# Optimization experiments

Hardware: AMD Instinct MI355X
Metric: run time of the kernel (lower is better)

Reference implementation:

```python
import jax, jax.numpy as jnp
import numpy as np

N_MEL = 80; ARNN = 1024; ADIM = 128; EMB = 512; PRE = 256; DRNN = 1024; NF = 32; KS = 31
B = 32; NCTX = 512; T = 500
PAD = (KS - 1) // 2


def setup_inputs() -> dict:
    key = jax.random.key(0)
    ks = jax.random.split(key, 20)
    g = lambda k, shape: jax.random.normal(k, shape, dtype=jnp.float32) * 0.02
    return {
        "memory": jax.random.normal(ks[0], (B, NCTX, EMB), dtype=jnp.float32),
        "decoder_inputs": jax.random.normal(ks[1], (B, N_MEL, T), dtype=jnp.float32),
        "mask": jnp.zeros((B, NCTX), dtype=bool),
        "prenet_w1": g(ks[2], (PRE, N_MEL)),
        "prenet_w2": g(ks[3], (PRE, PRE)),
        "arnn_wih": g(ks[4], (4 * ARNN, PRE + EMB)),
        "arnn_whh": g(ks[5], (4 * ARNN, ARNN)),
        "arnn_bih": jnp.zeros((4 * ARNN,), jnp.float32),
        "arnn_bhh": jnp.zeros((4 * ARNN,), jnp.float32),
        "q_w": g(ks[6], (ADIM, ARNN)),
        "m_w": g(ks[7], (ADIM, EMB)),
        "loc_conv_w": g(ks[8], (NF, 2, KS)),
        "loc_w": g(ks[9], (ADIM, NF)),
        "v_w": g(ks[10], (ADIM,)),
        "drnn_wih": g(ks[11], (4 * DRNN, ARNN + EMB)),
        "drnn_whh": g(ks[12], (4 * DRNN, DRNN)),
        "drnn_bih": jnp.zeros((4 * DRNN,), jnp.float32),
        "drnn_bhh": jnp.zeros((4 * DRNN,), jnp.float32),
        "proj_w": g(ks[13], (N_MEL, DRNN + EMB)),
        "proj_b": jnp.zeros((N_MEL,), jnp.float32),
        "gate_w": g(ks[14], (1, DRNN + EMB)),
        "gate_b": jnp.zeros((1,), jnp.float32),
    }


def _lstm_cell(x, h, c, wih, whh, bih, bhh):
    # PyTorch LSTMCell gate order: i, f, g, o
    z = x @ wih.T + h @ whh.T + bih + bhh
    i, f, g, o = jnp.split(z, 4, axis=-1)
    c2 = jax.nn.sigmoid(f) * c + jax.nn.sigmoid(i) * jnp.tanh(g)
    h2 = jax.nn.sigmoid(o) * jnp.tanh(c2)
    return h2, c2


def reference(memory, decoder_inputs, mask,
              prenet_w1, prenet_w2,
              arnn_wih, arnn_whh, arnn_bih, arnn_bhh,
              q_w, m_w, loc_conv_w, loc_w, v_w,
              drnn_wih, drnn_whh, drnn_bih, drnn_bhh,
              proj_w, proj_b, gate_w, gate_b):
    b, n_ctx, emb = memory.shape
    n_mel, t_out = decoder_inputs.shape[1], decoder_inputs.shape[2]

    # (time, batch, n_mel) with a leading zero go-frame; PreNet (eval: no dropout)
    x = jnp.transpose(decoder_inputs, (2, 0, 1))
    x = jnp.concatenate([jnp.zeros((1, b, n_mel), x.dtype), x], axis=0)
    h = jax.nn.relu(x @ prenet_w1.T)
    h = jax.nn.relu(h @ prenet_w2.T)  # (T+1, B, PRE)
    inputs = h[:-1]  # T decoder steps

    proc_mem = memory @ m_w.T  # (B, n_ctx, ADIM)

    def step(carry, xin):
        ah, ac, dh, dc, aw, awc, actx = carry
        cell_in = jnp.concatenate([xin, actx], axis=-1)
        ah, ac = _lstm_cell(cell_in, ah, ac, arnn_wih, arnn_whh, arnn_bih, arnn_bhh)
        # location-sensitive attention
        aw_cat = jnp.stack([aw, awc], axis=1)  # (B, 2, n_ctx)
        loc = jax.lax.conv_general_dilated(
            aw_cat, loc_conv_w, window_strides=(1,), padding=[(PAD, PAD)],
            dimension_numbers=("NCH", "OIH", "NCH"))  # (B, NF, n_ctx)
        loc = jnp.transpose(loc, (0, 2, 1)) @ loc_w.T  # (B, n_ctx, ADIM)
        q = (ah @ q_w.T)[:, None, :]  # (B, 1, ADIM)
        e = jnp.tanh(q + proc_mem + loc) @ v_w  # (B, n_ctx)
        e = jnp.where(mask, -1e9, e)
        aw = jax.nn.softmax(e, axis=-1)
        actx = jnp.einsum("bn,bne->be", aw, memory)
        awc = awc + aw
        din = jnp.concatenate([ah, actx], axis=-1)
        dh, dc = _lstm_cell(din, dh, dc, drnn_wih, drnn_whh, drnn_bih, drnn_bhh)
        dhc = jnp.concatenate([dh, actx], axis=-1)
        mel = dhc @ proj_w.T + proj_b  # (B, n_mel)
        gate = dhc @ gate_w.T + gate_b  # (B, 1)
        return (ah, ac, dh, dc, aw, awc, actx), (mel, gate[:, 0])

    z32 = lambda *s: jnp.zeros(s, memory.dtype)
    carry0 = (z32(b, ARNN), z32(b, ARNN), z32(b, DRNN), z32(b, DRNN),
              z32(b, n_ctx), z32(b, n_ctx), z32(b, emb))
    _, (mels, gates) = jax.lax.scan(step, carry0, inputs)
    mel_out = jnp.transpose(mels, (1, 2, 0))   # (B, n_mel, T)
    gate_out = jnp.transpose(gates, (1, 0))    # (B, T)
    return mel_out, gate_out
```

## Files before the change

kernel.cpp:

```cpp
#include <hip/hip_runtime.h>

#define NBLK 256
#define NTHR 512

constexpr int kNMel = 80, kArnn = 1024, kAdim = 128, kEmb = 512, kPre = 256;
constexpr int kNF = 32, kKS = 31, kB = 32, kNctx = 512, kT = 500, kPad = 15;

constexpr int KT_A = 56;
constexpr int KT_D = 80;
constexpr int KT_ALL = KT_A + KT_D;

constexpr int OFF_PREB   = 0;
constexpr int OFF_PROCMB = OFF_PREB + kT * kB * kPre / 2;
constexpr int OFF_QWTB   = OFF_PROCMB + kB * kNctx * kAdim / 2;
constexpr int OFF_LWT    = OFF_QWTB + kAdim * kArnn / 2;
constexpr int OFF_STATE  = OFF_LWT + kAdim * 33;
constexpr int OFF_AHB    = OFF_STATE;
constexpr int OFF_DHB    = OFF_AHB + 2 * kB * kArnn / 2;
constexpr int OFF_DH     = OFF_DHB + 2 * kB * kArnn / 2;
constexpr int OFF_AC     = OFF_DH + 2 * kB * kArnn;
constexpr int OFF_DC     = OFF_AC + kB * kArnn;
constexpr int OFF_ACTX   = OFF_DC + kB * kArnn;
constexpr int OFF_AW     = OFF_ACTX + kB * kEmb;
constexpr int OFF_AWC    = OFF_AW + kB * kNctx;
constexpr int OFF_PAW    = OFF_AWC + kB * kNctx;
constexpr int OFF_NUM    = OFF_PAW + kB * kNctx;
constexpr int OFF_DEN    = OFF_NUM + 2 * kB * kEmb;
constexpr int OFF_END    = OFF_DEN + 2 * kB;
constexpr int STATE_SZ   = OFF_END - OFF_STATE;
constexpr int OFF_BAR    = OFF_END;
constexpr int BAR_LINES  = 266;
constexpr int OFF_PAN    = OFF_BAR + BAR_LINES * 32;
constexpr int PAN_SZ     = NBLK * KT_ALL * 256;
constexpr int OFF_GMB    = OFF_PAN + PAN_SZ;
constexpr int GMB_SZ     = kB * kNctx * kEmb / 2;

typedef __attribute__((ext_vector_type(4))) float fvec4;
typedef __attribute__((ext_vector_type(8))) short bh8_t;
typedef unsigned long long u64;
typedef unsigned short ushortt;

union U64u { u64 u; float2 f2; ushortt s[4]; };

union SMem {
  struct { ushortt xs[8][2][2048]; } x1;
  struct { float zra[4][2][64][4]; float zrd[4][2][64][4];
           float hb[2][32][4]; } x2;
  struct { float ahb_s[kArnn]; float vw_s[kAdim]; float psum[512]; float q_s[kAdim];
           float aw_s[96]; float awc_s[96]; float cw[kNF * 2 * kKS];
           float loc_s[64 * 33]; float p_s[64]; float lwt[kAdim * 33];
           float dhc[kArnn + kEmb]; float pprj[126];
           ushortt pm[64 * kAdim]; } b;
  struct { float x8[8][80]; float h1[8][256]; } p;
  struct { float mem_s[4][512]; } m;
};

__device__ __forceinline__ float sigf(float x) { return 1.0f / (1.0f + __expf(-x)); }
__device__ __forceinline__ float tanhfast(float x) { return 1.0f - 2.0f / (__expf(2.0f * x) + 1.0f); }

__device__ __forceinline__ ushortt bf16rn(float f) {
  unsigned u = __float_as_uint(f);
  unsigned r = (u + 0x7FFFu + ((u >> 16) & 1u)) >> 16;
  return (ushortt)r;
}
__device__ __forceinline__ float bf2f(ushortt v) {
  return __uint_as_float((unsigned)v << 16);
}

__device__ __forceinline__ u64 ald64(const void* p) {
  return __hip_atomic_load((const u64*)p, __ATOMIC_RELAXED, __HIP_MEMORY_SCOPE_AGENT);
}
__device__ __forceinline__ float alf(const float* p) {
  return __hip_atomic_load(p, __ATOMIC_RELAXED, __HIP_MEMORY_SCOPE_AGENT);
}
__device__ __forceinline__ void asf(float* p, float v) {
  __hip_atomic_store(p, v, __ATOMIC_RELAXED, __HIP_MEMORY_SCOPE_AGENT);
}
__device__ __forceinline__ void as64(void* p, u64 v) {
  __hip_atomic_store((u64*)p, v, __ATOMIC_RELAXED, __HIP_MEMORY_SCOPE_AGENT);
}
__device__ __forceinline__ unsigned alu(const unsigned* p) {
  return __hip_atomic_load(p, __ATOMIC_RELAXED, __HIP_MEMORY_SCOPE_AGENT);
}
__device__ __forceinline__ void asu(unsigned* p, unsigned v) {
  __hip_atomic_store(p, v, __ATOMIC_RELAXED, __HIP_MEMORY_SCOPE_AGENT);
}

__device__ __forceinline__ void gbar_full(unsigned* cnt, unsigned* gen, unsigned& genv) {
  __syncthreads();
  if (threadIdx.x == 0) {
    __threadfence();
    unsigned arrived = __hip_atomic_fetch_add(cnt, 1u, __ATOMIC_ACQ_REL, __HIP_MEMORY_SCOPE_AGENT) + 1u;
    if (arrived == (unsigned)NBLK) {
      __hip_atomic_store(cnt, 0u, __ATOMIC_RELAXED, __HIP_MEMORY_SCOPE_AGENT);
      __hip_atomic_fetch_add(gen, 1u, __ATOMIC_ACQ_REL, __HIP_MEMORY_SCOPE_AGENT);
    } else {
      while (__hip_atomic_load(gen, __ATOMIC_ACQUIRE, __HIP_MEMORY_SCOPE_AGENT) == genv) {
        __builtin_amdgcn_s_sleep(2);
      }
    }
    ++genv;
  }
  __syncthreads();
}

__device__ __forceinline__ void gbar_light(unsigned* bar, unsigned target, int bk, int tid) {
  asm volatile("s_waitcnt vmcnt(0) lgkmcnt(0)" ::: "memory");
  __syncthreads();
  if (bk == 0) {
    if (tid < 64) {
      if (tid == 0) {
        asm volatile("s_waitcnt vmcnt(0)" ::: "memory");
      }
      unsigned i1 = (unsigned)tid * 4 + 1, i2 = i1 + 1, i3 = i1 + 2;
      unsigned i0 = (unsigned)tid * 4;
      for (;;) {
        bool ok = true;
        if (i0 != 0) ok = ok && (alu(&bar[i0 * 32]) >= target);
        ok = ok && (alu(&bar[i1 * 32]) >= target);
        ok = ok && (alu(&bar[i2 * 32]) >= target);
        ok = ok && (alu(&bar[i3 * 32]) >= target);
        if (__all(ok)) break;
        __builtin_amdgcn_s_sleep(1);
      }
      if (tid < 8) asu(&bar[(256 + tid) * 32], target);
    }
  } else {
    if (tid == 0) {
      asm volatile("s_waitcnt vmcnt(0)" ::: "memory");
      asu(&bar[bk * 32], target);
      unsigned* wk = &bar[(256 + (bk & 7)) * 32];
      while (alu(wk) < target) __builtin_amdgcn_s_sleep(1);
    }
  }
  __syncthreads();
}

template<int LS, int W>
__device__ __forceinline__ void lstm_wave(
    const ushortt* __restrict__ s0, const ushortt* __restrict__ s2,
    const float* __restrict__ numq, const float* __restrict__ invden,
    const short* __restrict__ pan,
    int l, ushortt* xstg, fvec4& z0, fvec4& z1)
{
  constexpr int NC  = LS ? 10 : 7;
  constexpr int CB  = LS ? W * 640 : W * 448;
  constexpr int KT0 = LS ? W * 20 : W * 14;
  constexpr int BD0 = LS ? 1024 : 256;
  constexpr int BD1 = LS ? 1536 : 768;
  const int u8 = l & 15, rj = l >> 4;
  const int m = l & 15, kg = l >> 4;

  u64 L0[8], L1[8];
  bh8_t f00, f01, f10, f11;

  auto load = [&](int c, u64* L, bh8_t& f0, bh8_t& f1) {
    const int c0 = CB + c * 64;
    if (c0 >= BD0 && c0 < BD1) {
      const float* base = numq + (c0 - BD0) + u8 * 4;
      #pragma unroll
      for (int j = 0; j < 8; ++j) {
        int row = 4 * j + rj;
        const float* fp = base + (size_t)row * kEmb;
        U64u a, b2; a.u = ald64(fp); b2.u = ald64(fp + 2);
        float s = invden[row];
        U64u pk;
        pk.s[0] = bf16rn(a.f2.x * s);  pk.s[1] = bf16rn(a.f2.y * s);
        pk.s[2] = bf16rn(b2.f2.x * s); pk.s[3] = bf16rn(b2.f2.y * s);
        L[j] = pk.u;
      }
    } else {
      const ushortt* bsrc; int stride; bool coh;
      if (c0 < BD0) { bsrc = s0 + c0;       stride = (LS ? 1024 : 256); coh = (LS == 1); }
      else          { bsrc = s2 + c0 - BD1; stride = 1024;              coh = true; }
      #pragma unroll
      for (int j = 0; j < 8; ++j) {
        const ushortt* ap = bsrc + (size_t)(4 * j + rj) * stride + u8 * 4;
        L[j] = coh ? ald64(ap) : *reinterpret_cast<const u64*>(ap);
      }
    }
    f0 = *reinterpret_cast<const bh8_t*>(pan + (size_t)(KT0 + c * 2) * 512 + l * 8);
    f1 = *reinterpret_cast<const bh8_t*>(pan + (size_t)(KT0 + c * 2 + 1) * 512 + l * 8);
  };
  auto stash = [&](int buf, u64* L) {
    #pragma unroll
    for (int j = 0; j < 8; ++j) {
      int row = 4 * j + rj;
      int sw = u8 ^ ((row & 7) << 1);
      *reinterpret_cast<u64*>(xstg + buf * 2048 + row * 64 + sw * 4) = L[j];
    }
  };
  auto consume = [&](int buf, bh8_t f0, bh8_t f1) {
    #pragma unroll
    for (int kt = 0; kt < 2; ++kt) {
      int sw = (2 * (kt * 4 + kg)) ^ ((m & 7) << 1);
      bh8_t a0 = *reinterpret_cast<const bh8_t*>(xstg + buf * 2048 + m * 64 + sw * 4);
      bh8_t a1 = *reinterpret_cast<const bh8_t*>(xstg + buf * 2048 + (16 + m) * 64 + sw * 4);
      bh8_t f = kt ? f1 : f0;
      z0 = __builtin_amdgcn_mfma_f32_16x16x32_bf16(a0, f, z0, 0, 0, 0);
      z1 = __builtin_amdgcn_mfma_f32_16x16x32_bf16(a1, f, z1, 0, 0, 0);
    }
  };

  load(0, L0, f00, f01);
  #pragma unroll
  for (int c = 0; c < NC; c += 2) {
    stash(0, L0);
    if (c + 1 < NC) load(c + 1, L1, f10, f11);
    consume(0, f00, f01);
    if (c + 1 < NC) {
      stash(1, L1);
      if (c + 2 < NC) load(c + 2, L0, f00, f01);
      consume(1, f10, f11);
    }
  }
}

extern "C" __global__ void __launch_bounds__(NTHR, 1)
decoder_kernel(const float* __restrict__ gmem, const float* __restrict__ dec,
               const unsigned char* __restrict__ mask,
               const float* __restrict__ pw1, const float* __restrict__ pw2,
               const float* __restrict__ awih, const float* __restrict__ awhh,
               const float* __restrict__ abih, const float* __restrict__ abhh,
               const float* __restrict__ qw, const float* __restrict__ mw,
               const float* __restrict__ cvw, const float* __restrict__ locw,
               const float* __restrict__ vw,
               const float* __restrict__ dwih, const float* __restrict__ dwhh,
               const float* __restrict__ dbih, const float* __restrict__ dbhh,
               const float* __restrict__ pjw, const float* __restrict__ pjb,
               const float* __restrict__ gw, const float* __restrict__ gb,
               float* __restrict__ out, float* __restrict__ ws, int useg)
{
  __shared__ SMem sm;
  __shared__ float s_invden[32];
  const int bk = blockIdx.x, tid = threadIdx.x;
  unsigned genv_f = 0, bcnt = 0;
  unsigned* bar = reinterpret_cast<unsigned*>(ws + OFF_BAR);
  unsigned* cntF = &bar[264 * 32];
  unsigned* genF = &bar[265 * 32];

  ushortt* PREBu = reinterpret_cast<ushortt*>(ws + OFF_PREB);
  ushortt* PROCMBu = reinterpret_cast<ushortt*>(ws + OFF_PROCMB);
  ushortt* QWTBu = reinterpret_cast<ushortt*>(ws + OFF_QWTB);
  float* LWT = ws + OFF_LWT;
  ushortt* AHBu = reinterpret_cast<ushortt*>(ws + OFF_AHB);
  ushortt* DHBu = reinterpret_cast<ushortt*>(ws + OFF_DHB);
  float* DH = ws + OFF_DH;
  float* AC = ws + OFF_AC;
  float* DC = ws + OFF_DC;
  float* ACTX = ws + OFF_ACTX;
  float* AWp = ws + OFF_AW;
  float* AWC = ws + OFF_AWC;
  float* PAW = ws + OFF_PAW;
  float* NUM = ws + OFF_NUM;
  float* DEN = ws + OFF_DEN;
  short* PANS = reinterpret_cast<short*>(ws + OFF_PAN);
  ushortt* GMB = reinterpret_cast<ushortt*>(ws + OFF_GMB);

  for (int i = bk * NTHR + tid; i < STATE_SZ; i += NBLK * NTHR) (ws + OFF_STATE)[i] = 0.f;
  for (int i = bk * NTHR + tid; i < kAdim * kArnn; i += NBLK * NTHR)
    QWTBu[i] = bf16rn(qw[i]);
  for (int i = bk * NTHR + tid; i < kAdim * kNF; i += NBLK * NTHR) {
    int d = i >> 5, f = i & 31;
    LWT[d * 33 + f] = locw[i];
  }
  gbar_full(cntF, genF, genv_f);

  if (bk == 0 && tid < 2 * kB) asf(&DEN[tid], 1.0f);
  for (int it = 0; it < 16; ++it) {
    int task0 = bk * 64 + it * 4;
    for (int i = tid; i < 2048; i += NTHR) {
      int pr = i >> 9, h = i & 511;
      sm.m.mem_s[pr][h] = gmem[(size_t)(task0 + pr) * kEmb + h];
    }
    __syncthreads();
    {
      int pr = tid >> 7, d = tid & 127;
      const float* mwr = mw + d * kEmb;
      float acc = 0.f;
      for (int h = 0; h < kEmb; ++h) acc = fmaf(sm.m.mem_s[pr][h], mwr[h], acc);
      PROCMBu[(size_t)(task0 + pr) * kAdim + d] = bf16rn(acc);
    }
    if (useg) {
      for (int i = tid; i < 2048; i += NTHR) {
        int pr = i >> 9, h = i & 511;
        GMB[(size_t)(task0 + pr) * kEmb + h] = bf16rn(sm.m.mem_s[pr][h]);
      }
    }
    __syncthreads();
  }
  for (int g = bk; g < 2000; g += NBLK) {
    int t_idx = g >> 2;
    int b0 = (g & 3) * 8;
    if (t_idx == 0) {
      for (int i = tid; i < 8 * kPre; i += NTHR)
        PREBu[(size_t)(b0 + (i >> 8)) * kPre + (i & 255)] = 0;
      continue;
    }
    for (int i = tid; i < 640; i += NTHR) {
      int bb = i / 80, m2 = i % 80;
      sm.p.x8[bb][m2] = dec[((size_t)(b0 + bb) * kNMel + m2) * kT + (t_idx - 1)];
    }
    __syncthreads();
    {
      int u = tid & 255, rep = tid >> 8;
      float acc[4] = {0.f, 0.f, 0.f, 0.f};
      for (int m2 = 0; m2 < 80; ++m2) {
        float w = pw1[u * kNMel + m2];
        #pragma unroll
        for (int r = 0; r < 4; ++r) acc[r] = fmaf(w, sm.p.x8[rep * 4 + r][m2], acc[r]);
      }
      #pragma unroll
      for (int r = 0; r < 4; ++r) sm.p.h1[rep * 4 + r][u] = fmaxf(acc[r], 0.f);
    }
    __syncthreads();
    {
      int u = tid & 255, rep = tid >> 8;
      float acc[4] = {0.f, 0.f, 0.f, 0.f};
      for (int k = 0; k < kPre; ++k) {
        float w = pw2[u * kPre + k];
        #pragma unroll
        for (int r = 0; r < 4; ++r) acc[r] = fmaf(w, sm.p.h1[rep * 4 + r][k], acc[r]);
      }
      #pragma unroll
      for (int r = 0; r < 4; ++r)
        PREBu[((size_t)t_idx * kB + b0 + rep * 4 + r) * kPre + u] = bf16rn(fmaxf(acc[r], 0.f));
    }
    __syncthreads();
  }
  {
    const int UNITS = NBLK * KT_ALL * 64;
    for (int u = bk * NTHR + tid; u < UNITS; u += NBLK * NTHR) {
      int bkk = u / (KT_ALL * 64);
      int rem = u - bkk * (KT_ALL * 64);
      int kta = rem >> 6, l = rem & 63;
      int lstm = (kta >= KT_A);
      int kt = lstm ? kta - KT_A : kta;
      int n = l & 15, kg = l >> 4;
      int r = (n >> 2) * 1024 + bkk * 4 + (n & 3);
      bh8_t v;
      #pragma unroll
      for (int j = 0; j < 8; ++j) {
        int k = kt * 32 + kg * 8 + j;
        float wv;
        if (!lstm) wv = (k < 768) ? awih[(size_t)r * 768 + k] : awhh[(size_t)r * 1024 + (k - 768)];
        else       wv = (k < 1536) ? dwih[(size_t)r * 1536 + k] : dwhh[(size_t)r * 1024 + (k - 1536)];
        v[j] = (short)bf16rn(wv);
      }
      *reinterpret_cast<bh8_t*>(PANS + (size_t)u * 8) = v;
    }
  }
  gbar_full(cntF, genF, genv_f);

  for (int t = 0; t <= kT; ++t) {
    const int p = t & 1, q = p ^ 1;
    float* nump = NUM + p * kB * kEmb;
    const float* numq = NUM + q * kB * kEmb;

    if (tid < kB) s_invden[tid] = 1.0f / alf(DEN + q * kB + tid);
    __syncthreads();
    if (t > 0 && tid < 64) {
      int idx = bk * 64 + tid;
      int b2 = idx >> 9;
      float invd = s_invden[b2];
      float av = PAW[idx] * invd;
      asf(&AWp[idx], av);
      asf(&AWC[idx], alf(&AWC[idx]) + av);
      asf(&ACTX[idx], alf(&numq[idx]) * invd);
    }
    if (t < kT) {
      if (tid < 64) asf(&nump[bk * 64 + tid], 0.f);
      if (bk == 0 && tid < kB) asf(DEN + p * kB + tid, 0.f);
    }
    {
      const int w8 = tid >> 6, l = tid & 63;
      fvec4 z0 = {0.f, 0.f, 0.f, 0.f}, z1 = z0;
      const ushortt* AHBq_ = AHBu + q * kB * kArnn;
      const ushortt* DHBp_ = DHBu + p * kB * kArnn;
      const ushortt* preb_t = PREBu + (size_t)t * kB * kPre;
      ushortt* xst = &sm.x1.xs[w8][0][0];
      const short* panb = PANS + (size_t)bk * (KT_ALL * 512);
      const short* pand = panb + KT_A * 512;
      if (w8 < 4) {
        if (t < kT) {
          switch (w8) {
            case 0: lstm_wave<0,0>(preb_t, AHBq_, numq, s_invden, panb, l, xst, z0, z1); break;
            case 1: lstm_wave<0,1>(preb_t, AHBq_, numq, s_invden, panb, l, xst, z0, z1); break;
            case 2: lstm_wave<0,2>(preb_t, AHBq_, numq, s_invden, panb, l, xst, z0, z1); break;
            default: lstm_wave<0,3>(preb_t, AHBq_, numq, s_invden, panb, l, xst, z0, z1); break;
          }
        }
      } else {
        if (t > 0) {
          switch (w8) {
            case 4: lstm_wave<1,0>(AHBq_, DHBp_, numq, s_invden, pand, l, xst, z0, z1); break;
            case 5: lstm_wave<1,1>(AHBq_, DHBp_, numq, s_invden, pand, l, xst, z0, z1); break;
            case 6: lstm_wave<1,2>(AHBq_, DHBp_, numq, s_invden, pand, l, xst, z0, z1); break;
            default: lstm_wave<1,3>(AHBq_, DHBp_, numq, s_invden, pand, l, xst, z0, z1); break;
          }
        }
      }
      __syncthreads();
      if (w8 < 4) {
        *reinterpret_cast<fvec4*>(&sm.x2.zra[w8][0][l][0]) = z0;
        *reinterpret_cast<fvec4*>(&sm.x2.zra[w8][1][l][0]) = z1;
      } else {
        *reinterpret_cast<fvec4*>(&sm.x2.zrd[w8 - 4][0][l][0]) = z0;
        *reinterpret_cast<fvec4*>(&sm.x2.zrd[w8 - 4][1][l][0]) = z1;
      }
    }
    __syncthreads();
    if (tid < 256) {
      const int ls = tid >> 7, uu = (tid >> 5) & 3, b = tid & 31;
      const bool go = (ls == 0) ? (t < kT) : (t > 0);
      if (go) {
        const int mt = b >> 4, mm = b & 15;
        const int lane_base = (mm >> 2) * 16, rr = mm & 3;
        float zg[4];
        #pragma unroll
        for (int g = 0; g < 4; ++g) {
          int ln = lane_base + g * 4 + uu;
          float s;
          if (ls == 0)
            s = sm.x2.zra[0][mt][ln][rr] + sm.x2.zra[1][mt][ln][rr]
              + sm.x2.zra[2][mt][ln][rr] + sm.x2.zra[3][mt][ln][rr];
          else
            s = sm.x2.zrd[0][mt][ln][rr] + sm.x2.zrd[1][mt][ln][rr]
              + sm.x2.zrd[2][mt][ln][rr] + sm.x2.zrd[3][mt][ln][rr];
          int rg = g * 1024 + bk * 4 + uu;
          s += (ls ? dbih[rg] + dbhh[rg] : abih[rg] + abhh[rg]);
          zg[g] = s;
        }
        float* cst = ls ? DC : AC;
        const int idx = b * kArnn + bk * 4 + uu;
        float c = sigf(zg[1]) * cst[idx] + sigf(zg[0]) * tanhfast(zg[2]);
        cst[idx] = c;
        float h = sigf(zg[3]) * tanhfast(c);
        if (ls) asf(&DH[q * kB * kArnn + idx], h);
        sm.x2.hb[ls][b][uu] = h;
      }
    }
    __syncthreads();
    if (tid < 64) {
      int ls = tid >> 5, b = tid & 31;
      bool go2 = ls ? (t > 0) : (t < kT);
      if (go2) {
        U64u pk;
        #pragma unroll
        for (int j = 0; j < 4; ++j) pk.s[j] = bf16rn(sm.x2.hb[ls][b][j]);
        ushortt* dst = (ls ? (DHBu + q * kB * kArnn) : (AHBu + p * kB * kArnn)) + b * kArnn + bk * 4;
        as64(dst, pk.u);
      }
    }
    gbar_light(bar, ++bcnt, bk, tid);

    if (t < kT) {
      const int b = bk >> 3, sub = bk & 7, j0 = sub * 64;
      const int pbase = (sub == 0) ? 0 : 21 + (sub - 1) * 20;
      const int pcnt = (sub == 0) ? 21 : 20;
      const ushortt* AHBp_ = AHBu + p * kB * kArnn;
      if (tid < 256) {
        U64u v; v.u = ald64(AHBp_ + b * kArnn + tid * 4);
        #pragma unroll
        for (int j = 0; j < 4; ++j) sm.b.ahb_s[tid * 4 + j] = bf2f(v.s[j]);
      }
      for (int i = tid; i < 94; i += NTHR) {
        int jj = j0 - kPad + i;
        bool ok = (jj >= 0 && jj < kNctx);
        sm.b.aw_s[i] = ok ? alf(&AWp[b * kNctx + jj]) : 0.f;
        sm.b.awc_s[i] = ok ? alf(&AWC[b * kNctx + jj]) : 0.f;
      }
      for (int i = tid; i < kNF * 2 * kKS; i += NTHR) sm.b.cw[i] = cvw[i];
      for (int i = tid; i < kAdim * 33; i += NTHR) sm.b.lwt[i] = LWT[i];
      for (int i = tid; i < kAdim; i += NTHR) sm.b.vw_s[i] = vw[i];
      {
        const fvec4* src = reinterpret_cast<const fvec4*>(PROCMBu + (size_t)(b * kNctx + j0) * kAdim);
        fvec4* dst = reinterpret_cast<fvec4*>(sm.b.pm);
        for (int i = tid; i < 1024; i += NTHR) dst[i] = src[i];
      }
      if (sub < 4 && t > 0) {
        for (int i = tid; i < kArnn + kEmb; i += NTHR)
          sm.b.dhc[i] = (i < kArnn) ? alf(&DH[q * kB * kArnn + b * kArnn + i])
                                    : alf(&ACTX[b * kEmb + (i - kArnn)]);
      }
      __syncthreads();
      {
        int d = tid & 127, qr = tid >> 7;
        const ushortt* wq = QWTBu + (size_t)d * kArnn + qr * 256;
        const float* ahs = sm.b.ahb_s + qr * 256;
        float acc = 0.f;
        #pragma unroll 4
        for (int h8 = 0; h8 < 32; ++h8) {
          U64u a, c2;
          a.u = *reinterpret_cast<const u64*>(wq + h8 * 8);
          c2.u = *reinterpret_cast<const u64*>(wq + h8 * 8 + 4);
          #pragma unroll
          for (int j = 0; j < 4; ++j) acc = fmaf(bf2f(a.s[j]), ahs[h8 * 8 + j], acc);
          #pragma unroll
          for (int j = 0; j < 4; ++j) acc = fmaf(bf2f(c2.s[j]), ahs[h8 * 8 + 4 + j], acc);
        }
        sm.b.psum[tid] = acc;
      }
      __syncthreads();
      if (tid < kAdim)
        sm.b.q_s[tid] = sm.b.psum[tid] + sm.b.psum[128 + tid]
                      + sm.b.psum[256 + tid] + sm.b.psum[384 + tid];
      {
        int j = tid >> 3, f0 = (tid & 7) * 4;
        #pragma unroll
        for (int fi = 0; fi < 4; ++fi) {
          int f = f0 + fi;
          const float* w0 = &sm.b.cw[f * 62];
          float s = 0.f;
          for (int k = 0; k < kKS; ++k)
            s = fmaf(sm.b.aw_s[j + k], w0[k], fmaf(sm.b.awc_s[j + k], w0[31 + k], s));
          sm.b.loc_s[j * 33 + f] = s;
        }
      }
      if (sub < 4 && t > 0 && tid < pcnt * 6) {
        int ol = tid / 6, kc = tid % 6, og = pbase + ol;
        const float* row = (og < kNMel) ? pjw + (size_t)og * (kArnn + kEmb) : gw;
        const float* x = sm.b.dhc + kc * 256;
        const float* r2 = row + kc * 256;
        float acc = 0.f;
        for (int k = 0; k < 256; ++k) acc = fmaf(r2[k], x[k], acc);
        sm.b.pprj[tid] = acc;
      }
      __syncthreads();
      {
        int j = tid >> 3, grp = tid & 7, jj = j0 + j;
        float pe = 0.f;
        #pragma unroll 4
        for (int dd = 0; dd < 16; ++dd) {
          int d = grp + 8 * dd;
          float l2 = 0.f;
          const float* ls2 = &sm.b.loc_s[j * 33];
          const float* lw2 = &sm.b.lwt[d * 33];
          #pragma unroll 8
          for (int f = 0; f < kNF; ++f) l2 = fmaf(ls2[f], lw2[f], l2);
          float x = sm.b.q_s[d] + bf2f(sm.b.pm[j * kAdim + d]) + l2;
          pe = fmaf(sm.b.vw_s[d], tanhfast(x), pe);
        }
        pe += __shfl_xor(pe, 1);
        pe += __shfl_xor(pe, 2);
        pe += __shfl_xor(pe, 4);
        if (grp == 0) {
          float pv = mask[b * kNctx + jj] ? 0.f : __expf(pe);
          sm.b.p_s[j] = pv;
          PAW[b * kNctx + jj] = pv;
        }
      }
      if (sub < 4 && t > 0 && tid < pcnt) {
        int og = pbase + tid;
        float val = (og < kNMel) ? pjb[og] : gb[0];
        #pragma unroll
        for (int kc = 0; kc < 6; ++kc) val += sm.b.pprj[tid * 6 + kc];
        if (og < kNMel) out[((size_t)b * kNMel + og) * kT + (t - 1)] = val;
        else out[(size_t)kB * kNMel * kT + b * kT + (t - 1)] = val;
      }
      __syncthreads();
      if (tid < 64) {
        float v = sm.b.p_s[tid];
        #pragma unroll
        for (int o = 1; o < 64; o <<= 1) v += __shfl_xor(v, o);
        if (tid == 0) atomicAdd(DEN + p * kB + b, v);
      }
      if (useg) {
        const ushortt* memb = GMB + (size_t)(b * kNctx + j0) * kEmb + tid;
        float a0 = 0.f, a1 = 0.f, a2 = 0.f, a3 = 0.f;
        #pragma unroll 4
        for (int jj2 = 0; jj2 < 64; jj2 += 4) {
          a0 = fmaf(sm.b.p_s[jj2],     bf2f(memb[(size_t)jj2 * kEmb]), a0);
          a1 = fmaf(sm.b.p_s[jj2 + 1], bf2f(memb[(size_t)(jj2 + 1) * kEmb]), a1);
          a2 = fmaf(sm.b.p_s[jj2 + 2], bf2f(memb[(size_t)(jj2 + 2) * kEmb]), a2);
          a3 = fmaf(sm.b.p_s[jj2 + 3], bf2f(memb[(size_t)(jj2 + 3) * kEmb]), a3);
        }
        atomicAdd(&nump[b * kEmb + tid], (a0 + a1) + (a2 + a3));
      } else {
        const float* memb = gmem + (size_t)(b * kNctx + j0) * kEmb + tid;
        float a0 = 0.f, a1 = 0.f;
        #pragma unroll 8
        for (int jj2 = 0; jj2 < 64; jj2 += 2) {
          a0 = fmaf(sm.b.p_s[jj2], memb[(size_t)jj2 * kEmb], a0);
          a1 = fmaf(sm.b.p_s[jj2 + 1], memb[(size_t)(jj2 + 1) * kEmb], a1);
        }
        atomicAdd(&nump[b * kEmb + tid], a0 + a1);
      }
      gbar_light(bar, ++bcnt, bk, tid);
    }
  }

  if (bk < kB) {
    const int b = bk;
    for (int i = tid; i < kArnn + kEmb; i += NTHR)
      sm.b.dhc[i] = (i < kArnn) ? alf(&DH[1 * kB * kArnn + b * kArnn + i])
                                : alf(&ACTX[b * kEmb + (i - kArnn)]);
    __syncthreads();
    if (tid < 486) {
      int ol = tid / 6, kc = tid % 6;
      const float* row = (ol < kNMel) ? pjw + (size_t)ol * (kArnn + kEmb) : gw;
      const float* x = sm.b.dhc + kc * 256;
      const float* r2 = row + kc * 256;
      float acc = 0.f;
      for (int k = 0; k < 256; ++k) acc = fmaf(r2[k], x[k], acc);
      sm.b.psum[tid] = acc;
    }
    __syncthreads();
    if (tid < 81) {
      float val = (tid < kNMel) ? pjb[tid] : gb[0];
      #pragma unroll
      for (int kc = 0; kc < 6; ++kc) val += sm.b.psum[tid * 6 + kc];
      if (tid < kNMel) out[((size_t)b * kNMel + tid) * kT + (kT - 1)] = val;
      else out[(size_t)kB * kNMel * kT + b * kT + (kT - 1)] = val;
    }
  }
}

extern "C" void kernel_launch(void* const* d_in, const int* in_sizes, int n_in,
                              void* d_out, int out_size, void* d_ws, size_t ws_size,
                              hipStream_t stream) {
  const float* gmem = (const float*)d_in[0];
  const float* dec = (const float*)d_in[1];
  const unsigned char* mask = (const unsigned char*)d_in[2];
  const float* pw1 = (const float*)d_in[3];
  const float* pw2 = (const float*)d_in[4];
  const float* awih = (const float*)d_in[5];
  const float* awhh = (const float*)d_in[6];
  const float* abih = (const float*)d_in[7];
  const float* abhh = (const float*)d_in[8];
  const float* qw = (const float*)d_in[9];
  const float* mw = (const float*)d_in[10];
  const float* cvw = (const float*)d_in[11];
  const float* locw = (const float*)d_in[12];
  const float* vw = (const float*)d_in[13];
  const float* dwih = (const float*)d_in[14];
  const float* dwhh = (const float*)d_in[15];
  const float* dbih = (const float*)d_in[16];
  const float* dbhh = (const float*)d_in[17];
  const float* pjw = (const float*)d_in[18];
  const float* pjb = (const float*)d_in[19];
  const float* gw = (const float*)d_in[20];
  const float* gb = (const float*)d_in[21];
  float* out = (float*)d_out;
  float* ws = (float*)d_ws;

  int useg = (ws_size >= (size_t)(OFF_GMB + GMB_SZ) * sizeof(float)) ? 1 : 0;

  hipMemsetAsync((char*)d_ws + (size_t)OFF_BAR * sizeof(float), 0,
                 (size_t)BAR_LINES * 128, stream);
  hipLaunchKernelGGL(decoder_kernel, dim3(NBLK), dim3(NTHR), 0, stream,
                     gmem, dec, mask, pw1, pw2, awih, awhh, abih, abhh, qw, mw,
                     cvw, locw, vw, dwih, dwhh, dbih, dbhh, pjw, pjb, gw, gb,
                     out, ws, useg);
}
```

Measured before the change: 38.91 ms.

## Stage shared LSTM activations once per block in LDS instead of per-wave

```diff
diff --git a/kernel.cpp b/kernel.cpp
--- a/kernel.cpp
+++ b/kernel.cpp
@@ -42,8 +42,12 @@
 
 union U64u { u64 u; float2 f2; ushortt s[4]; };
 
+constexpr int AH_O = 0;
+constexpr int DH_O = 16384;
+constexpr int AX_O = 32768;
+
 union SMem {
-  struct { ushortt xs[8][2][2048]; } x1;
+  struct { ushortt stage[49152]; } x1;
   struct { float zra[4][2][64][4]; float zrd[4][2][64][4];
            float hb[2][32][4]; } x2;
   struct { float ahb_s[kArnn]; float vw_s[kAdim]; float psum[512]; float q_s[kAdim];
@@ -109,11 +113,8 @@
   __syncthreads();
   if (bk == 0) {
     if (tid < 64) {
-      if (tid == 0) {
-        asm volatile("s_waitcnt vmcnt(0)" ::: "memory");
-      }
-      unsigned i1 = (unsigned)tid * 4 + 1, i2 = i1 + 1, i3 = i1 + 2;
-      unsigned i0 = (unsigned)tid * 4;
+      if (tid == 0) asm volatile("s_waitcnt vmcnt(0)" ::: "memory");
+      unsigned i0 = (unsigned)tid * 4, i1 = i0 + 1, i2 = i0 + 2, i3 = i0 + 3;
       for (;;) {
         bool ok = true;
         if (i0 != 0) ok = ok && (alu(&bar[i0 * 32]) >= target);
@@ -136,83 +137,130 @@
   __syncthreads();
 }
 
-template<int LS, int W>
-__device__ __forceinline__ void lstm_wave(
-    const ushortt* __restrict__ s0, const ushortt* __restrict__ s2,
-    const float* __restrict__ numq, const float* __restrict__ invden,
-    const short* __restrict__ pan,
-    int l, ushortt* xstg, fvec4& z0, fvec4& z1)
+__device__ __forceinline__ void stage_half1(int tid, const ushortt* __restrict__ AHBq,
+    const ushortt* __restrict__ DHBp, const float* __restrict__ numq,
+    const float* __restrict__ invden, ushortt* __restrict__ lds)
 {
-  constexpr int NC  = LS ? 10 : 7;
-  constexpr int CB  = LS ? W * 640 : W * 448;
-  constexpr int KT0 = LS ? W * 20 : W * 14;
-  constexpr int BD0 = LS ? 1024 : 256;
-  constexpr int BD1 = LS ? 1536 : 768;
-  const int u8 = l & 15, rj = l >> 4;
+  const int uc = tid & 127;
+  const int r0 = tid >> 7;
+  const int chunk = uc >> 4, u8c = uc & 15;
+  u64 va[8], vd[8], ax[8];
+  #pragma unroll
+  for (int i = 0; i < 8; ++i) {
+    int row = r0 + 4 * i;
+    va[i] = ald64(AHBq + (size_t)row * 1024 + uc * 4);
+    vd[i] = ald64(DHBp + (size_t)row * 1024 + uc * 4);
+  }
+  #pragma unroll
+  for (int i = 0; i < 8; ++i) {
+    int row = r0 + 4 * i;
+    const float* np = numq + (size_t)row * 512 + uc * 4;
+    U64u a, b; a.u = ald64(np); b.u = ald64(np + 2);
+    float s = invden[row];
+    U64u pk;
+    pk.s[0] = bf16rn(a.f2.x * s);  pk.s[1] = bf16rn(a.f2.y * s);
+    pk.s[2] = bf16rn(b.f2.x * s);  pk.s[3] = bf16rn(b.f2.y * s);
+    ax[i] = pk.u;
+  }
+  #pragma unroll
+  for (int i = 0; i < 8; ++i) {
+    int row = r0 + 4 * i;
+    int sw = u8c ^ ((row & 7) << 1);
+    int off = chunk * 2048 + row * 64 + sw * 4;
+    *reinterpret_cast<u64*>(lds + AH_O + off) = va[i];
+    *reinterpret_cast<u64*>(lds + DH_O + off) = vd[i];
+    *reinterpret_cast<u64*>(lds + AX_O + off) = ax[i];
+  }
+}
+__device__ __forceinline__ void load_half2(int tid, const ushortt* __restrict__ AHBq,
+    const ushortt* __restrict__ DHBp, u64* va, u64* vd)
+{
+  const int uc = tid & 127, r0 = tid >> 7;
+  #pragma unroll
+  for (int i = 0; i < 8; ++i) {
+    int row = r0 + 4 * i;
+    va[i] = ald64(AHBq + (size_t)row * 1024 + 512 + uc * 4);
+    vd[i] = ald64(DHBp + (size_t)row * 1024 + 512 + uc * 4);
+  }
+}
+__device__ __forceinline__ void write_half2(int tid, const u64* va, const u64* vd,
+                                            ushortt* __restrict__ lds)
+{
+  const int uc = tid & 127, r0 = tid >> 7;
+  const int chunk = uc >> 4, u8c = uc & 15;
+  #pragma unroll
+  for (int i = 0; i < 8; ++i) {
+    int row = r0 + 4 * i;
+    int sw = u8c ^ ((row & 7) << 1);
+    int off = chunk * 2048 + row * 64 + sw * 4;
+    *reinterpret_cast<u64*>(lds + AH_O + off) = va[i];
+    *reinterpret_cast<u64*>(lds + DH_O + off) = vd[i];
+  }
+}
+
+__device__ constexpr int lds_base(int LS, int kt) {
+  if (LS == 0) {
+    if (kt < 24) return AX_O + ((kt - 8) >> 1) * 2048;
+    if (kt < 40) return AH_O + ((kt - 24) >> 1) * 2048;
+    return AH_O + ((kt - 40) >> 1) * 2048;
+  } else {
+    if (kt < 16) return AH_O + (kt >> 1) * 2048;
+    if (kt < 32) return AH_O + ((kt - 16) >> 1) * 2048;
+    if (kt < 48) return AX_O + ((kt - 32) >> 1) * 2048;
+    if (kt < 64) return DH_O + ((kt - 48) >> 1) * 2048;
+    return DH_O + ((kt - 64) >> 1) * 2048;
+  }
+}
+
+template<int LS, int W, int HALF>
+__device__ __forceinline__ void consume(const ushortt* __restrict__ lds,
+    const short* __restrict__ pan, const ushortt* __restrict__ preb_t,
+    int l, fvec4& z0, fvec4& z1)
+{
   const int m = l & 15, kg = l >> 4;
-
-  u64 L0[8], L1[8];
-  bh8_t f00, f01, f10, f11;
-
-  auto load = [&](int c, u64* L, bh8_t& f0, bh8_t& f1) {
-    const int c0 = CB + c * 64;
-    if (c0 >= BD0 && c0 < BD1) {
-      const float* base = numq + (c0 - BD0) + u8 * 4;
-      #pragma unroll
-      for (int j = 0; j < 8; ++j) {
-        int row = 4 * j + rj;
-        const float* fp = base + (size_t)row * kEmb;
-        U64u a, b2; a.u = ald64(fp); b2.u = ald64(fp + 2);
-        float s = invden[row];
-        U64u pk;
-        pk.s[0] = bf16rn(a.f2.x * s);  pk.s[1] = bf16rn(a.f2.y * s);
-        pk.s[2] = bf16rn(b2.f2.x * s); pk.s[3] = bf16rn(b2.f2.y * s);
-        L[j] = pk.u;
-      }
-    } else {
-      const ushortt* bsrc; int stride; bool coh;
-      if (c0 < BD0) { bsrc = s0 + c0;       stride = (LS ? 1024 : 256); coh = (LS == 1); }
-      else          { bsrc = s2 + c0 - BD1; stride = 1024;              coh = true; }
-      #pragma unroll
-      for (int j = 0; j < 8; ++j) {
-        const ushortt* ap = bsrc + (size_t)(4 * j + rj) * stride + u8 * 4;
-        L[j] = coh ? ald64(ap) : *reinterpret_cast<const u64*>(ap);
-      }
-    }
-    f0 = *reinterpret_cast<const bh8_t*>(pan + (size_t)(KT0 + c * 2) * 512 + l * 8);
-    f1 = *reinterpret_cast<const bh8_t*>(pan + (size_t)(KT0 + c * 2 + 1) * 512 + l * 8);
+  bh8_t fA[4], fB[4], fC[4];
+  auto ld4 = [&](int kt0, bh8_t* f) {
+    #pragma unroll
+    for (int i = 0; i < 4; ++i)
+      f[i] = *reinterpret_cast<const bh8_t*>(pan + (size_t)(kt0 + i) * 512 + l * 8);
   };
-  auto stash = [&](int buf, u64* L) {
+  auto run4 = [&](int kt0, bh8_t* f) {
     #pragma unroll
-    for (int j = 0; j < 8; ++j) {
-      int row = 4 * j + rj;
-      int sw = u8 ^ ((row & 7) << 1);
-      *reinterpret_cast<u64*>(xstg + buf * 2048 + row * 64 + sw * 4) = L[j];
+    for (int i = 0; i < 4; ++i) {
+      const int kt = kt0 + i;
+      const int base = lds_base(LS, kt);
+      const int sw = (2 * ((kt & 1) * 4 + kg)) ^ ((m & 7) << 1);
+      bh8_t a0 = *reinterpret_cast<const bh8_t*>(lds + base + m * 64 + sw * 4);
+      bh8_t a1 = *reinterpret_cast<const bh8_t*>(lds + base + (16 + m) * 64 + sw * 4);
+      z0 = __builtin_amdgcn_mfma_f32_16x16x32_bf16(a0, f[i], z0, 0, 0, 0);
+      z1 = __builtin_amdgcn_mfma_f32_16x16x32_bf16(a1, f[i], z1, 0, 0, 0);
     }
   };
-  auto consume = [&](int buf, bh8_t f0, bh8_t f1) {
+  if constexpr (LS == 0 && HALF == 0) {
+    ld4(8 + 4 * W, fA); ld4(24 + 4 * W, fB);
+    run4(8 + 4 * W, fA); run4(24 + 4 * W, fB);
+  } else if constexpr (LS == 0 && HALF == 1) {
+    bh8_t p0[2], p1[2], pf[2];
     #pragma unroll
-    for (int kt = 0; kt < 2; ++kt) {
-      int sw = (2 * (kt * 4 + kg)) ^ ((m & 7) << 1);
-      bh8_t a0 = *reinterpret_cast<const bh8_t*>(xstg + buf * 2048 + m * 64 + sw * 4);
-      bh8_t a1 = *reinterpret_cast<const bh8_t*>(xstg + buf * 2048 + (16 + m) * 64 + sw * 4);
-      bh8_t f = kt ? f1 : f0;
-      z0 = __builtin_amdgcn_mfma_f32_16x16x32_bf16(a0, f, z0, 0, 0, 0);
-      z1 = __builtin_amdgcn_mfma_f32_16x16x32_bf16(a1, f, z1, 0, 0, 0);
-    }
-  };
-
-  load(0, L0, f00, f01);
-  #pragma unroll
-  for (int c = 0; c < NC; c += 2) {
-    stash(0, L0);
-    if (c + 1 < NC) load(c + 1, L1, f10, f11);
-    consume(0, f00, f01);
-    if (c + 1 < NC) {
-      stash(1, L1);
-      if (c + 2 < NC) load(c + 2, L0, f00, f01);
-      consume(1, f10, f11);
-    }
+    for (int i = 0; i < 2; ++i) {
+      const int kt = 2 * W + i;
+      p0[i] = *reinterpret_cast<const bh8_t*>(preb_t + (size_t)m * 256 + kt * 32 + kg * 8);
+      p1[i] = *reinterpret_cast<const bh8_t*>(preb_t + (size_t)(16 + m) * 256 + kt * 32 + kg * 8);
+      pf[i] = *reinterpret_cast<const bh8_t*>(pan + (size_t)kt * 512 + l * 8);
+    }
+    ld4(40 + 4 * W, fA);
+    #pragma unroll
+    for (int i = 0; i < 2; ++i) {
+      z0 = __builtin_amdgcn_mfma_f32_16x16x32_bf16(p0[i], pf[i], z0, 0, 0, 0);
+      z1 = __builtin_amdgcn_mfma_f32_16x16x32_bf16(p1[i], pf[i], z1, 0, 0, 0);
+    }
+    run4(40 + 4 * W, fA);
+  } else if constexpr (LS == 1 && HALF == 0) {
+    ld4(4 * W, fA); ld4(32 + 4 * W, fB); ld4(48 + 4 * W, fC);
+    run4(4 * W, fA); run4(32 + 4 * W, fB); run4(48 + 4 * W, fC);
+  } else {
+    ld4(16 + 4 * W, fA); ld4(64 + 4 * W, fB);
+    run4(16 + 4 * W, fA); run4(64 + 4 * W, fB);
   }
 }
 
@@ -356,6 +404,8 @@
     const int p = t & 1, q = p ^ 1;
     float* nump = NUM + p * kB * kEmb;
     const float* numq = NUM + q * kB * kEmb;
+    const ushortt* AHBq_ = AHBu + q * kB * kArnn;
+    const ushortt* DHBp_ = DHBu + p * kB * kArnn;
 
     if (tid < kB) s_invden[tid] = 1.0f / alf(DEN + q * kB + tid);
     __syncthreads();
@@ -373,31 +423,49 @@
       if (bk == 0 && tid < kB) asf(DEN + p * kB + tid, 0.f);
     }
     {
+      ushortt* XL = reinterpret_cast<ushortt*>(&sm);
+      stage_half1(tid, AHBq_, DHBp_, numq, s_invden, XL);
+      u64 vA2[8], vD2[8];
+      load_half2(tid, AHBq_, DHBp_, vA2, vD2);
+      __syncthreads();
       const int w8 = tid >> 6, l = tid & 63;
       fvec4 z0 = {0.f, 0.f, 0.f, 0.f}, z1 = z0;
-      const ushortt* AHBq_ = AHBu + q * kB * kArnn;
-      const ushortt* DHBp_ = DHBu + p * kB * kArnn;
       const ushortt* preb_t = PREBu + (size_t)t * kB * kPre;
-      ushortt* xst = &sm.x1.xs[w8][0][0];
       const short* panb = PANS + (size_t)bk * (KT_ALL * 512);
       const short* pand = panb + KT_A * 512;
-      if (w8 < 4) {
-        if (t < kT) {
-          switch (w8) {
-            case 0: lstm_wave<0,0>(preb_t, AHBq_, numq, s_invden, panb, l, xst, z0, z1); break;
-            case 1: lstm_wave<0,1>(preb_t, AHBq_, numq, s_invden, panb, l, xst, z0, z1); break;
-            case 2: lstm_wave<0,2>(preb_t, AHBq_, numq, s_invden, panb, l, xst, z0, z1); break;
-            default: lstm_wave<0,3>(preb_t, AHBq_, numq, s_invden, panb, l, xst, z0, z1); break;
-          }
-        }
-      } else {
-        if (t > 0) {
-          switch (w8) {
-            case 4: lstm_wave<1,0>(AHBq_, DHBp_, numq, s_invden, pand, l, xst, z0, z1); break;
-            case 5: lstm_wave<1,1>(AHBq_, DHBp_, numq, s_invden, pand, l, xst, z0, z1); break;
-            case 6: lstm_wave<1,2>(AHBq_, DHBp_, numq, s_invden, pand, l, xst, z0, z1); break;
-            default: lstm_wave<1,3>(AHBq_, DHBp_, numq, s_invden, pand, l, xst, z0, z1); break;
-          }
+      const bool aA = (w8 < 4) && (t < kT);
+      const bool aD = (w8 >= 4) && (t > 0);
+      if (aA) {
+        switch (w8) {
+          case 0: consume<0, 0, 0>(XL, panb, preb_t, l, z0, z1); break;
+          case 1: consume<0, 1, 0>(XL, panb, preb_t, l, z0, z1); break;
+          case 2: consume<0, 2, 0>(XL, panb, preb_t, l, z0, z1); break;
+          default: consume<0, 3, 0>(XL, panb, preb_t, l, z0, z1); break;
+        }
+      } else if (aD) {
+        switch (w8) {
+          case 4: consume<1, 0, 0>(XL, pand, preb_t, l, z0, z1); break;
+          case 5: consume<1, 1, 0>(XL, pand, preb_t, l, z0, z1); break;
+          case 6: consume<1, 2, 0>(XL, pand, preb_t, l, z0, z1); break;
+          default: consume<1, 3, 0>(XL, pand, preb_t, l, z0, z1); break;
+        }
+      }
+      __syncthreads();
+      write_half2(tid, vA2, vD2, XL);
+      __syncthreads();
+      if (aA) {
+        switch (w8) {
+          case 0: consume<0, 0, 1>(XL, panb, preb_t, l, z0, z1); break;
+          case 1: consume<0, 1, 1>(XL, panb, preb_t, l, z0, z1); break;
+          case 2: consume<0, 2, 1>(XL, panb, preb_t, l, z0, z1); break;
+          default: consume<0, 3, 1>(XL, panb, preb_t, l, z0, z1); break;
+        }
+      } else if (aD) {
+        switch (w8) {
+          case 4: consume<1, 0, 1>(XL, pand, preb_t, l, z0, z1); break;
+          case 5: consume<1, 1, 1>(XL, pand, preb_t, l, z0, z1); break;
+          case 6: consume<1, 2, 1>(XL, pand, preb_t, l, z0, z1); break;
+          default: consume<1, 3, 1>(XL, pand, preb_t, l, z0, z1); break;
         }
       }
       __syncthreads();
```

Measured after the change: 39.91 ms. 2.6% more time.

## Replicate recurrent hidden states per XCD and precompute attention-context tile in LDS

Applied to the files above, without the earlier changes.

```diff
diff --git a/kernel.cpp b/kernel.cpp
--- a/kernel.cpp
+++ b/kernel.cpp
@@ -29,10 +29,13 @@
 constexpr int OFF_END    = OFF_DEN + 2 * kB;
 constexpr int STATE_SZ   = OFF_END - OFF_STATE;
 constexpr int OFF_BAR    = OFF_END;
-constexpr int BAR_LINES  = 266;
+constexpr int BAR_LINES  = 282;
 constexpr int OFF_PAN    = OFF_BAR + BAR_LINES * 32;
 constexpr int PAN_SZ     = NBLK * KT_ALL * 256;
-constexpr int OFF_GMB    = OFF_PAN + PAN_SZ;
+constexpr int SLOT_USH   = 131072;
+constexpr int OFF_SLOT   = OFF_PAN + PAN_SZ;
+constexpr int SLOT_SZF   = 2 * 8 * SLOT_USH / 2;
+constexpr int OFF_GMB    = OFF_SLOT + SLOT_SZF;
 constexpr int GMB_SZ     = kB * kNctx * kEmb / 2;
 
 typedef __attribute__((ext_vector_type(4))) float fvec4;
@@ -43,7 +46,7 @@
 union U64u { u64 u; float2 f2; ushortt s[4]; };
 
 union SMem {
-  struct { ushortt xs[8][2][2048]; } x1;
+  struct { ushortt ax[8 * 2048]; ushortt xs[8][2048]; } x1;
   struct { float zra[4][2][64][4]; float zrd[4][2][64][4];
            float hb[2][32][4]; } x2;
   struct { float ahb_s[kArnn]; float vw_s[kAdim]; float psum[512]; float q_s[kAdim];
@@ -84,6 +87,16 @@
 }
 __device__ __forceinline__ void asu(unsigned* p, unsigned v) {
   __hip_atomic_store(p, v, __ATOMIC_RELAXED, __HIP_MEMORY_SCOPE_AGENT);
+}
+
+__device__ __forceinline__ u64 ld64_sc0(const ushortt* p) {
+  u64 v;
+  asm volatile("global_load_dwordx2 %0, %1, off sc0" : "=v"(v) : "v"(p));
+  return v;
+}
+__device__ __forceinline__ void vm_drain() {
+  asm volatile("s_waitcnt vmcnt(0)" ::: "memory");
+  __builtin_amdgcn_sched_barrier(0);
 }
 
 __device__ __forceinline__ void gbar_full(unsigned* cnt, unsigned* gen, unsigned& genv) {
@@ -109,11 +122,8 @@
   __syncthreads();
   if (bk == 0) {
     if (tid < 64) {
-      if (tid == 0) {
-        asm volatile("s_waitcnt vmcnt(0)" ::: "memory");
-      }
-      unsigned i1 = (unsigned)tid * 4 + 1, i2 = i1 + 1, i3 = i1 + 2;
-      unsigned i0 = (unsigned)tid * 4;
+      if (tid == 0) asm volatile("s_waitcnt vmcnt(0)" ::: "memory");
+      unsigned i0 = (unsigned)tid * 4, i1 = i0 + 1, i2 = i0 + 2, i3 = i0 + 3;
       for (;;) {
         bool ok = true;
         if (i0 != 0) ok = ok && (alu(&bar[i0 * 32]) >= target);
@@ -138,80 +148,67 @@
 
 template<int LS, int W>
 __device__ __forceinline__ void lstm_wave(
-    const ushortt* __restrict__ s0, const ushortt* __restrict__ s2,
-    const float* __restrict__ numq, const float* __restrict__ invden,
-    const short* __restrict__ pan,
-    int l, ushortt* xstg, fvec4& z0, fvec4& z1)
+    const ushortt* __restrict__ preb_t,
+    const ushortt* __restrict__ slotAH, const ushortt* __restrict__ slotDH,
+    const ushortt* __restrict__ axl, const short* __restrict__ pan,
+    int l, ushortt* xs, fvec4& z0, fvec4& z1)
 {
   constexpr int NC  = LS ? 10 : 7;
   constexpr int CB  = LS ? W * 640 : W * 448;
   constexpr int KT0 = LS ? W * 20 : W * 14;
-  constexpr int BD0 = LS ? 1024 : 256;
-  constexpr int BD1 = LS ? 1536 : 768;
   const int u8 = l & 15, rj = l >> 4;
   const int m = l & 15, kg = l >> 4;
 
-  u64 L0[8], L1[8];
-  bh8_t f00, f01, f10, f11;
-
-  auto load = [&](int c, u64* L, bh8_t& f0, bh8_t& f1) {
+  #pragma unroll
+  for (int c = 0; c < NC; ++c) {
     const int c0 = CB + c * 64;
-    if (c0 >= BD0 && c0 < BD1) {
-      const float* base = numq + (c0 - BD0) + u8 * 4;
+    const int ktA = KT0 + 2 * c;
+    bh8_t f0 = *reinterpret_cast<const bh8_t*>(pan + (size_t)ktA * 512 + l * 8);
+    bh8_t f1 = *reinterpret_cast<const bh8_t*>(pan + (size_t)(ktA + 1) * 512 + l * 8);
+    const bool isAX = LS ? (c0 >= 1024 && c0 < 1536) : (c0 >= 256 && c0 < 768);
+    if (isAX) {
+      const int axch = LS ? ((c0 - 1024) >> 6) : ((c0 - 256) >> 6);
+      const ushortt* base = axl + axch * 2048;
+      #pragma unroll
+      for (int kt = 0; kt < 2; ++kt) {
+        int sw = (2 * (kt * 4 + kg)) ^ ((m & 7) << 1);
+        bh8_t a0 = *reinterpret_cast<const bh8_t*>(base + m * 64 + sw * 4);
+        bh8_t a1 = *reinterpret_cast<const bh8_t*>(base + (16 + m) * 64 + sw * 4);
+        bh8_t f = kt ? f1 : f0;
+        z0 = __builtin_amdgcn_mfma_f32_16x16x32_bf16(a0, f, z0, 0, 0, 0);
+        z1 = __builtin_amdgcn_mfma_f32_16x16x32_bf16(a1, f, z1, 0, 0, 0);
+      }
+    } else {
+      u64 L[8];
+      if (!LS && c0 < 256) {
+        const ushortt* bsrc = preb_t + c0;
+        #pragma unroll
+        for (int j = 0; j < 8; ++j)
+          L[j] = *reinterpret_cast<const u64*>(bsrc + (size_t)(4 * j + rj) * 256 + u8 * 4);
+      } else {
+        const ushortt* bsrc;
+        if (LS) bsrc = (c0 < 1024) ? (slotAH + c0) : (slotDH + (c0 - 1536));
+        else    bsrc = slotAH + (c0 - 768);
+        #pragma unroll
+        for (int j = 0; j < 8; ++j)
+          L[j] = ld64_sc0(bsrc + (size_t)(4 * j + rj) * 1024 + u8 * 4);
+        vm_drain();
+      }
       #pragma unroll
       for (int j = 0; j < 8; ++j) {
         int row = 4 * j + rj;
-        const float* fp = base + (size_t)row * kEmb;
-        U64u a, b2; a.u = ald64(fp); b2.u = ald64(fp + 2);
-        float s = invden[row];
-        U64u pk;
-        pk.s[0] = bf16rn(a.f2.x * s);  pk.s[1] = bf16rn(a.f2.y * s);
-        pk.s[2] = bf16rn(b2.f2.x * s); pk.s[3] = bf16rn(b2.f2.y * s);
-        L[j] = pk.u;
-      }
-    } else {
-      const ushortt* bsrc; int stride; bool coh;
-      if (c0 < BD0) { bsrc = s0 + c0;       stride = (LS ? 1024 : 256); coh = (LS == 1); }
-      else          { bsrc = s2 + c0 - BD1; stride = 1024;              coh = true; }
+        int sw = u8 ^ ((row & 7) << 1);
+        *reinterpret_cast<u64*>(xs + row * 64 + sw * 4) = L[j];
+      }
       #pragma unroll
-      for (int j = 0; j < 8; ++j) {
-        const ushortt* ap = bsrc + (size_t)(4 * j + rj) * stride + u8 * 4;
-        L[j] = coh ? ald64(ap) : *reinterpret_cast<const u64*>(ap);
-      }
-    }
-    f0 = *reinterpret_cast<const bh8_t*>(pan + (size_t)(KT0 + c * 2) * 512 + l * 8);
-    f1 = *reinterpret_cast<const bh8_t*>(pan + (size_t)(KT0 + c * 2 + 1) * 512 + l * 8);
-  };
-  auto stash = [&](int buf, u64* L) {
-    #pragma unroll
-    for (int j = 0; j < 8; ++j) {
-      int row = 4 * j + rj;
-      int sw = u8 ^ ((row & 7) << 1);
-      *reinterpret_cast<u64*>(xstg + buf * 2048 + row * 64 + sw * 4) = L[j];
-    }
-  };
-  auto consume = [&](int buf, bh8_t f0, bh8_t f1) {
-    #pragma unroll
-    for (int kt = 0; kt < 2; ++kt) {
-      int sw = (2 * (kt * 4 + kg)) ^ ((m & 7) << 1);
-      bh8_t a0 = *reinterpret_cast<const bh8_t*>(xstg + buf * 2048 + m * 64 + sw * 4);
-      bh8_t a1 = *reinterpret_cast<const bh8_t*>(xstg + buf * 2048 + (16 + m) * 64 + sw * 4);
-      bh8_t f = kt ? f1 : f0;
-      z0 = __builtin_amdgcn_mfma_f32_16x16x32_bf16(a0, f, z0, 0, 0, 0);
-      z1 = __builtin_amdgcn_mfma_f32_16x16x32_bf16(a1, f, z1, 0, 0, 0);
-    }
-  };
-
-  load(0, L0, f00, f01);
-  #pragma unroll
-  for (int c = 0; c < NC; c += 2) {
-    stash(0, L0);
-    if (c + 1 < NC) load(c + 1, L1, f10, f11);
-    consume(0, f00, f01);
-    if (c + 1 < NC) {
-      stash(1, L1);
-      if (c + 2 < NC) load(c + 2, L0, f00, f01);
-      consume(1, f10, f11);
+      for (int kt = 0; kt < 2; ++kt) {
+        int sw = (2 * (kt * 4 + kg)) ^ ((m & 7) << 1);
+        bh8_t a0 = *reinterpret_cast<const bh8_t*>(xs + m * 64 + sw * 4);
+        bh8_t a1 = *reinterpret_cast<const bh8_t*>(xs + (16 + m) * 64 + sw * 4);
+        bh8_t f = kt ? f1 : f0;
+        z0 = __builtin_amdgcn_mfma_f32_16x16x32_bf16(a0, f, z0, 0, 0, 0);
+        z1 = __builtin_amdgcn_mfma_f32_16x16x32_bf16(a1, f, z1, 0, 0, 0);
+      }
     }
   }
 }
@@ -233,11 +230,16 @@
 {
   __shared__ SMem sm;
   __shared__ float s_invden[32];
+  __shared__ int s_chunk;
   const int bk = blockIdx.x, tid = threadIdx.x;
   unsigned genv_f = 0, bcnt = 0;
   unsigned* bar = reinterpret_cast<unsigned*>(ws + OFF_BAR);
   unsigned* cntF = &bar[264 * 32];
   unsigned* genF = &bar[265 * 32];
+
+  unsigned myxcd;
+  asm("s_getreg_b32 %0, hwreg(HW_REG_XCC_ID)" : "=s"(myxcd));
+  myxcd &= 7u;
 
   ushortt* PREBu = reinterpret_cast<ushortt*>(ws + OFF_PREB);
   ushortt* PROCMBu = reinterpret_cast<ushortt*>(ws + OFF_PROCMB);
@@ -255,9 +257,11 @@
   float* NUM = ws + OFF_NUM;
   float* DEN = ws + OFF_DEN;
   short* PANS = reinterpret_cast<short*>(ws + OFF_PAN);
+  ushortt* SLOTu = reinterpret_cast<ushortt*>(ws + OFF_SLOT);
   ushortt* GMB = reinterpret_cast<ushortt*>(ws + OFF_GMB);
 
   for (int i = bk * NTHR + tid; i < STATE_SZ; i += NBLK * NTHR) (ws + OFF_STATE)[i] = 0.f;
+  for (int i = bk * NTHR + tid; i < SLOT_SZF; i += NBLK * NTHR) (ws + OFF_SLOT)[i] = 0.f;
   for (int i = bk * NTHR + tid; i < kAdim * kArnn; i += NBLK * NTHR)
     QWTBu[i] = bf16rn(qw[i]);
   for (int i = bk * NTHR + tid; i < kAdim * kNF; i += NBLK * NTHR) {
@@ -372,31 +376,53 @@
       if (tid < 64) asf(&nump[bk * 64 + tid], 0.f);
       if (bk == 0 && tid < kB) asf(DEN + p * kB + tid, 0.f);
     }
+    if (bk == 0 && tid < 8) asu(&bar[(266 + q * 8 + tid) * 32], 0u);
+    {
+      ushortt* axl = sm.x1.ax;
+      for (int task = tid; task < 2048; task += NTHR) {
+        int ch = task >> 8, r = (task >> 3) & 31, g8 = task & 7;
+        const float* np = numq + (size_t)r * 512 + ch * 64 + g8 * 8;
+        float s = s_invden[r];
+        U64u a, b2, c2, d2;
+        a.u = ald64(np); b2.u = ald64(np + 2); c2.u = ald64(np + 4); d2.u = ald64(np + 6);
+        U64u p0, p1;
+        p0.s[0] = bf16rn(a.f2.x * s);  p0.s[1] = bf16rn(a.f2.y * s);
+        p0.s[2] = bf16rn(b2.f2.x * s); p0.s[3] = bf16rn(b2.f2.y * s);
+        p1.s[0] = bf16rn(c2.f2.x * s); p1.s[1] = bf16rn(c2.f2.y * s);
+        p1.s[2] = bf16rn(d2.f2.x * s); p1.s[3] = bf16rn(d2.f2.y * s);
+        ushortt* base = axl + ch * 2048 + r * 64;
+        int x = (r & 7) << 1;
+        *reinterpret_cast<u64*>(base + ((2 * g8) ^ x) * 4) = p0.u;
+        *reinterpret_cast<u64*>(base + ((2 * g8 + 1) ^ x) * 4) = p1.u;
+      }
+    }
+    __syncthreads();
     {
       const int w8 = tid >> 6, l = tid & 63;
       fvec4 z0 = {0.f, 0.f, 0.f, 0.f}, z1 = z0;
-      const ushortt* AHBq_ = AHBu + q * kB * kArnn;
-      const ushortt* DHBp_ = DHBu + p * kB * kArnn;
+      const ushortt* slotAH = SLOTu + ((size_t)p * 8 + myxcd) * SLOT_USH;
+      const ushortt* slotDH = slotAH + 65536;
       const ushortt* preb_t = PREBu + (size_t)t * kB * kPre;
-      ushortt* xst = &sm.x1.xs[w8][0][0];
       const short* panb = PANS + (size_t)bk * (KT_ALL * 512);
       const short* pand = panb + KT_A * 512;
+      ushortt* xs = &sm.x1.xs[w8][0];
+      ushortt* axl = sm.x1.ax;
       if (w8 < 4) {
         if (t < kT) {
           switch (w8) {
-            case 0: lstm_wave<0,0>(preb_t, AHBq_, numq, s_invden, panb, l, xst, z0, z1); break;
-            case 1: lstm_wave<0,1>(preb_t, AHBq_, numq, s_invden, panb, l, xst, z0, z1); break;
-            case 2: lstm_wave<0,2>(preb_t, AHBq_, numq, s_invden, panb, l, xst, z0, z1); break;
-            default: lstm_wave<0,3>(preb_t, AHBq_, numq, s_invden, panb, l, xst, z0, z1); break;
+            case 0: lstm_wave<0,0>(preb_t, slotAH, slotDH, axl, panb, l, xs, z0, z1); break;
+            case 1: lstm_wave<0,1>(preb_t, slotAH, slotDH, axl, panb, l, xs, z0, z1); break;
+            case 2: lstm_wave<0,2>(preb_t, slotAH, slotDH, axl, panb, l, xs, z0, z1); break;
+            default: lstm_wave<0,3>(preb_t, slotAH, slotDH, axl, panb, l, xs, z0, z1); break;
           }
         }
       } else {
         if (t > 0) {
           switch (w8) {
-            case 4: lstm_wave<1,0>(AHBq_, DHBp_, numq, s_invden, pand, l, xst, z0, z1); break;
-            case 5: lstm_wave<1,1>(AHBq_, DHBp_, numq, s_invden, pand, l, xst, z0, z1); break;
-            case 6: lstm_wave<1,2>(AHBq_, DHBp_, numq, s_invden, pand, l, xst, z0, z1); break;
-            default: lstm_wave<1,3>(AHBq_, DHBp_, numq, s_invden, pand, l, xst, z0, z1); break;
+            case 4: lstm_wave<1,0>(preb_t, slotAH, slotDH, axl, pand, l, xs, z0, z1); break;
+            case 5: lstm_wave<1,1>(preb_t, slotAH, slotDH, axl, pand, l, xs, z0, z1); break;
+            case 6: lstm_wave<1,2>(preb_t, slotAH, slotDH, axl, pand, l, xs, z0, z1); break;
+            default: lstm_wave<1,3>(preb_t, slotAH, slotDH, axl, pand, l, xs, z0, z1); break;
           }
         }
       }
@@ -459,6 +485,11 @@
       const int pbase = (sub == 0) ? 0 : 21 + (sub - 1) * 20;
       const int pcnt = (sub == 0) ? 21 : 20;
       const ushortt* AHBp_ = AHBu + p * kB * kArnn;
+      if (tid == 0) {
+        unsigned a = __hip_atomic_fetch_add(&bar[(266 + q * 8 + (int)myxcd) * 32], 1u,
+                                            __ATOMIC_RELAXED, __HIP_MEMORY_SCOPE_AGENT);
+        s_chunk = (int)a;
+      }
       if (tid < 256) {
         U64u v; v.u = ald64(AHBp_ + b * kArnn + tid * 4);
         #pragma unroll
@@ -484,6 +515,17 @@
                                     : alf(&ACTX[b * kEmb + (i - kArnn)]);
       }
       __syncthreads();
+      if (s_chunk < 32) {
+        ushortt* sb = SLOTu + ((size_t)q * 8 + myxcd) * SLOT_USH;
+        if (tid < 256) {
+          u64 v = ald64(AHBu + (size_t)p * kB * kArnn + s_chunk * 1024 + tid * 4);
+          *reinterpret_cast<u64*>(sb + (size_t)s_chunk * 1024 + tid * 4) = v;
+        } else {
+          int j = tid - 256;
+          u64 v = ald64(DHBu + (size_t)q * kB * kArnn + s_chunk * 1024 + j * 4);
+          *reinterpret_cast<u64*>(sb + 65536 + (size_t)s_chunk * 1024 + j * 4) = v;
+        }
+      }
       {
         int d = tid & 127, qr = tid >> 7;
         const ushortt* wq = QWTBu + (size_t)d * kArnn + qr * 256;
```

New measurement: 39.28 ms. No clear change (+1.0%).
